# Optimization experiments

Measured on AMD Instinct MI355X. Metric: run time of the kernel, lower is better.

## Reference

```python
import jax, jax.numpy as jnp
import numpy as np

K = 3       # kernel_size
RATE = 2    # dilation rate
NH = 8      # num_heads
EPS = 1e-5  # InstanceNorm eps


def _conv1x1(x, W, b):
    # x: [B,C,H,W], W: [O,C], b: [O]
    return jnp.einsum('bchw,oc->bohw', x, W) + b[None, :, None, None]


def _inorm(x):
    mu = jnp.mean(x, axis=(2, 3), keepdims=True)
    var = jnp.var(x, axis=(2, 3), keepdims=True)
    return (x - mu) / jnp.sqrt(var + EPS)


def _extract_patches(x):
    # dilated KxK patches, stride 1, 'same' grid -> [B, C, K*K, H, W]
    B, C, H, W = x.shape
    pad = RATE * (K - 1) // 2
    xp = jnp.pad(x, ((0, 0), (0, 0), (pad, pad), (pad, pad)))
    taps = [xp[:, :, i * RATE:i * RATE + H, j * RATE:j * RATE + W]
            for i in range(K) for j in range(K)]
    return jnp.stack(taps, axis=2)


def setup_inputs() -> dict:
    key = jax.random.key(0)
    ks = jax.random.split(key, 8)
    B, C, H, W, A = 1, 64, 64, 64, 128
    features = jax.random.normal(ks[0], (B, C, H, W), jnp.float32)
    masks = jax.random.uniform(ks[1], (B, 1, H, W), jnp.float32)
    s_in = 1.0 / np.sqrt(C).astype(np.float32)
    Wq = jax.random.normal(ks[2], (A, C), jnp.float32) * s_in
    bq = jnp.zeros((A,), jnp.float32)
    Wk = jax.random.normal(ks[3], (A, C), jnp.float32) * s_in
    bk = jnp.zeros((A,), jnp.float32)
    Wo = jax.random.normal(ks[4], (C, C), jnp.float32) * s_in
    bo = jnp.zeros((C,), jnp.float32)
    return dict(features=features, masks=masks, Wq=Wq, bq=bq,
                Wk=Wk, bk=bk, Wo=Wo, bo=bo)


def reference(features, masks, Wq, bq, Wk, bk, Wo, bo):
    B, C, H, W = features.shape
    A = Wq.shape[0]
    hc = A // NH
    L = H * W
    KK = K * K

    m = (masks > 0.5).astype(features.dtype)          # 1 = hole
    f_masked = features * m
    f_unmasked = features * (1.0 - m)

    q = jax.nn.relu(_inorm(_conv1x1(f_masked, Wq, bq)))    # [B,A,H,W]
    k = jax.nn.relu(_inorm(_conv1x1(f_unmasked, Wk, bk)))  # [B,A,H,W]

    # per-head dilated patch banks: [B,NH,hc*KK,L]
    qp = _extract_patches(q).reshape(B, NH, hc * KK, L)
    kp = _extract_patches(k).reshape(B, NH, hc * KK, L)

    # patch-correlation attention per head: [B,NH,L,L]
    attn = jax.nn.softmax(jnp.einsum('bndq,bndk->bnqk', qp, kp), axis=-1)

    # value patch bank from unmasked features: [B,C*KK,L]
    vp = _extract_patches(f_unmasked).reshape(B, C * KK, L)

    # sample value patches: [B,NH,L,C*KK]
    sampled = jnp.einsum('bnqk,bdk->bnqd', attn, vp)

    # fold: average the KK taps per channel, then average over heads
    attended = sampled.reshape(B, NH, L, C, KK).mean(axis=4).mean(axis=1)  # [B,L,C]
    attended = attended.transpose(0, 2, 1).reshape(B, C, H, W)

    return jax.nn.relu(_inorm(_conv1x1(attended, Wo, bo)))
```

## Files before the change

### kernel.cpp

```cpp
#include <hip/hip_runtime.h>
#include <hip/hip_bf16.h>


#define LL 4096
#define CC 64
#define AA 128
#define NH_ 8
#define KSTR 144
#define LOG2E 1.44269504088896340736f

typedef _Float16 half8 __attribute__((ext_vector_type(8)));
typedef float floatx4 __attribute__((ext_vector_type(4)));
typedef int intx4 __attribute__((ext_vector_type(4)));

__device__ __forceinline__ float fexp2(float x) {
    float r;
    asm("v_exp_f32 %0, %1" : "=v"(r) : "v"(x));
    return r;
}

__global__ __launch_bounds__(512) void prep_kernel(
    const float* __restrict__ feat,
    const float* __restrict__ masks,
    const float* __restrict__ Wq, const float* __restrict__ bq,
    const float* __restrict__ Wk, const float* __restrict__ bk,
    _Float16* __restrict__ q_act, _Float16* __restrict__ k_act,
    _Float16* __restrict__ vb)
{
    const int tid = threadIdx.x;
    const int b = blockIdx.x;
    __shared__ float sWq[CC], sWk[CC];
    __shared__ float sm[32];

    if (b >= AA) {
        int c = b - AA;
        for (int p = 0; p < 8; ++p) {
            int l = p * 512 + tid;
            int y = l >> 6, x = l & 63;
            float s = 0.f;
            for (int ty = 0; ty < 3; ++ty) {
                int yy = y + 2 * (ty - 1);
                if (yy < 0 || yy > 63) continue;
                for (int tx = 0; tx < 3; ++tx) {
                    int xx = x + 2 * (tx - 1);
                    if (xx < 0 || xx > 63) continue;
                    int ll = yy * 64 + xx;
                    float hole = masks[ll] > 0.5f ? 1.f : 0.f;
                    s += feat[c * LL + ll] * (1.f - hole);
                }
            }
            vb[c * LL + l] = (_Float16)(s * (1.f / 9.f));
        }
        return;
    }

    const int a = b;
    if (tid < CC) {
        sWq[tid] = Wq[a * CC + tid];
        sWk[tid] = Wk[a * CC + tid];
    }
    __syncthreads();
    const float biasq = bq[a], biask = bk[a];

    float accq[8], acck[8];
#pragma unroll
    for (int p = 0; p < 8; ++p) { accq[p] = 0.f; acck[p] = 0.f; }
    for (int c = 0; c < CC; ++c) {
        float wq = sWq[c], wk = sWk[c];
        const float* fr = feat + (size_t)c * LL + tid;
#pragma unroll
        for (int p = 0; p < 8; ++p) {
            float f = fr[p * 512];
            accq[p] += wq * f;
            acck[p] += wk * f;
        }
    }

    float valsq[8], valsk[8];
    float s1q = 0.f, s2q = 0.f, s1k = 0.f, s2k = 0.f;
#pragma unroll
    for (int p = 0; p < 8; ++p) {
        int l = p * 512 + tid;
        float hole = masks[l] > 0.5f ? 1.f : 0.f;
        float vq = accq[p] * hole + biasq;
        float vk = acck[p] * (1.f - hole) + biask;
        valsq[p] = vq; s1q += vq; s2q += vq * vq;
        valsk[p] = vk; s1k += vk; s2k += vk * vk;
    }
    for (int off = 32; off; off >>= 1) {
        s1q += __shfl_down(s1q, off, 64);
        s2q += __shfl_down(s2q, off, 64);
        s1k += __shfl_down(s1k, off, 64);
        s2k += __shfl_down(s2k, off, 64);
    }
    int wv = tid >> 6, ln = tid & 63;
    if (ln == 0) {
        sm[wv * 4] = s1q; sm[wv * 4 + 1] = s2q;
        sm[wv * 4 + 2] = s1k; sm[wv * 4 + 3] = s2k;
    }
    __syncthreads();
    s1q = 0.f; s2q = 0.f; s1k = 0.f; s2k = 0.f;
#pragma unroll
    for (int i = 0; i < 8; ++i) {
        s1q += sm[i * 4]; s2q += sm[i * 4 + 1];
        s1k += sm[i * 4 + 2]; s2k += sm[i * 4 + 3];
    }
    float muq = s1q * (1.f / LL);
    float invq = rsqrtf(s2q * (1.f / LL) - muq * muq + 1e-5f);
    float muk = s1k * (1.f / LL);
    float invk = rsqrtf(s2k * (1.f / LL) - muk * muk + 1e-5f);

    _Float16* qa = q_act + (size_t)a * LL;
    _Float16* ka = k_act + (size_t)a * LL;
#pragma unroll
    for (int p = 0; p < 8; ++p) {
        int l = p * 512 + tid;
        float vq = (valsq[p] - muq) * invq;
        float vk = (valsk[p] - muk) * invk;
        qa[l] = (_Float16)(vq > 0.f ? vq * LOG2E : 0.f);
        ka[l] = (_Float16)(vk > 0.f ? vk : 0.f);
    }
}

__global__ __launch_bounds__(256) void build_kp(
    const _Float16* __restrict__ k_act, _Float16* __restrict__ kp)
{
    const int n = blockIdx.x, y = blockIdx.y;
    const int tid = threadIdx.x;
    const _Float16* ka = k_act + (size_t)n * 16 * LL;
    __shared__ _Float16 kt[16][3][72];

    for (int idx = tid; idx < 16 * 3 * 68; idx += 256) {
        int row = idx / 68, xr = idx - row * 68;
        int ah = row / 3, ty = row - ah * 3;
        int yy = y + 2 * (ty - 1);
        int xx = xr - 2;
        _Float16 v = (_Float16)0.f;
        if (yy >= 0 && yy <= 63 && xx >= 0 && xx <= 63)
            v = ka[ah * LL + yy * 64 + xx];
        kt[ah][ty][xr] = v;
    }
    __syncthreads();

    _Float16* base = kp + ((size_t)n * LL + y * 64) * KSTR;
#pragma unroll
    for (int i = 0; i < 5; ++i) {
        int idx = tid + i * 256;
        if (idx < 64 * 18) {
            int x = idx / 18, c18 = idx - x * 18;
            half8 v8;
#pragma unroll
            for (int j = 0; j < 8; ++j) {
                int d = c18 * 8 + j;
                int ah = d / 9, t = d - ah * 9;
                int ty = t / 3, tx = t - ty * 3;
                v8[j] = kt[ah][ty][x + 2 * tx];
            }
            *(half8*)(base + (size_t)idx * 8) = v8;
        }
    }
}

__global__ __launch_bounds__(256, 2) void attn_kernel(
    const _Float16* __restrict__ q_act, const _Float16* __restrict__ kp,
    const _Float16* __restrict__ vb,
    _Float16* __restrict__ Opart, float* __restrict__ ml)
{
    const int bid = blockIdx.x;
    const int n = bid & 7;
    const int slot = bid >> 3;
    const int qt2 = slot & 31;
    const int h = slot >> 5;
    const int jt0 = h * 32;
    const int tid = threadIdx.x;
    const int w = tid >> 6, lane = tid & 63;
    const int l15 = lane & 15, quad = lane >> 4;

    __shared__ __align__(16) _Float16 Bk[2][64 * KSTR + 16];

    if (tid < 32) Bk[tid >> 4][64 * KSTR + (tid & 15)] = (_Float16)0.f;

    const _Float16* kpn = kp + (size_t)n * LL * KSTR;

    auto issue_bk = [&](int jt, _Float16* dst) {
        const char* tile = (const char*)(kpn + (size_t)jt * 64 * KSTR) + (lane << 4);
        for (int c = w; c < 18; c += 4) {
            __builtin_amdgcn_global_load_lds(
                (const __attribute__((address_space(1))) void*)(tile + c * 1024),
                (__attribute__((address_space(3))) void*)(dst + c * 512),
                16, 0, 0);
        }
    };

    half8 afrag[2][5];
    {
        const _Float16* qa = q_act + (size_t)n * 16 * LL;
        const int x = w * 16 + l15;
#pragma unroll
        for (int rs = 0; rs < 2; ++rs) {
            const int y = qt2 * 2 + rs;
#pragma unroll
            for (int ks = 0; ks < 5; ++ks) {
#pragma unroll
                for (int j = 0; j < 8; ++j) {
                    int d = ks * 32 + quad * 8 + j;
                    _Float16 v = (_Float16)0.f;
                    if (d < 144) {
                        int ah = d / 9, t = d - ah * 9;
                        int ty = t / 3, tx = t - ty * 3;
                        int yy = y + 2 * (ty - 1);
                        int xx = x + 2 * (tx - 1);
                        if (yy >= 0 && yy <= 63 && xx >= 0 && xx <= 63)
                            v = qa[ah * LL + yy * 64 + xx];
                    }
                    afrag[rs][ks][j] = v;
                }
            }
        }
    }

    floatx4 accO[2][4];
    float mrow[2], lrow[2];
#pragma unroll
    for (int rs = 0; rs < 2; ++rs) {
        mrow[rs] = -1e30f; lrow[rs] = 0.f;
#pragma unroll
        for (int i = 0; i < 4; ++i) accO[rs][i] = (floatx4){0.f, 0.f, 0.f, 0.f};
    }

    const int aLo = (((quad & 1) << 5) + l15) << 2;
    const int aHi = aLo + 64;
    const bool selHi = (quad >> 1) != 0;

    const _Float16* vpl = vb + (size_t)l15 * LL + quad * 8;

    auto softmax_pack = [&](floatx4* accS, floatx4* accOr,
                            float& mr, float& lr, half8* pfr) {
        float t0 = fmaxf(fmaxf(accS[0][0], accS[0][1]), fmaxf(accS[0][2], accS[0][3]));
        float t1 = fmaxf(fmaxf(accS[1][0], accS[1][1]), fmaxf(accS[1][2], accS[1][3]));
        float t2 = fmaxf(fmaxf(accS[2][0], accS[2][1]), fmaxf(accS[2][2], accS[2][3]));
        float t3 = fmaxf(fmaxf(accS[3][0], accS[3][1]), fmaxf(accS[3][2], accS[3][3]));
        float tm = fmaxf(fmaxf(t0, t1), fmaxf(t2, t3));
        tm = fmaxf(tm, __shfl_xor(tm, 16, 64));
        tm = fmaxf(tm, __shfl_xor(tm, 32, 64));
        float mn = fmaxf(mr, tm);
        float alpha = fexp2(mr - mn);
        mr = mn;
        lr *= alpha;
        float af[4];
#pragma unroll
        for (int r = 0; r < 4; ++r) af[r] = __shfl(alpha, quad * 4 + r, 16);
#pragma unroll
        for (int nt = 0; nt < 4; ++nt)
#pragma unroll
            for (int r = 0; r < 4; ++r) accOr[nt][r] *= af[r];
        float rsum = 0.f;
#pragma unroll
        for (int nt = 0; nt < 4; ++nt)
#pragma unroll
            for (int r = 0; r < 4; ++r) {
                float pv = fexp2(accS[nt][r] - mn);
                accS[nt][r] = pv;
                rsum += pv;
            }
        lr += rsum;

        int pkw[4][2];
#pragma unroll
        for (int nt = 0; nt < 4; ++nt)
#pragma unroll
            for (int rp = 0; rp < 2; ++rp) {
                auto hp = __builtin_amdgcn_cvt_pkrtz(accS[nt][2 * rp],
                                                     accS[nt][2 * rp + 1]);
                pkw[nt][rp] = __builtin_bit_cast(int, hp);
            }
#pragma unroll
        for (int ks2 = 0; ks2 < 2; ++ks2) {
            int w0A = __builtin_amdgcn_ds_bpermute(aLo, pkw[2 * ks2][0]);
            int w0B = __builtin_amdgcn_ds_bpermute(aLo, pkw[2 * ks2 + 1][0]);
            int w1A = __builtin_amdgcn_ds_bpermute(aLo, pkw[2 * ks2][1]);
            int w1B = __builtin_amdgcn_ds_bpermute(aLo, pkw[2 * ks2 + 1][1]);
            int w2A = __builtin_amdgcn_ds_bpermute(aHi, pkw[2 * ks2][0]);
            int w2B = __builtin_amdgcn_ds_bpermute(aHi, pkw[2 * ks2 + 1][0]);
            int w3A = __builtin_amdgcn_ds_bpermute(aHi, pkw[2 * ks2][1]);
            int w3B = __builtin_amdgcn_ds_bpermute(aHi, pkw[2 * ks2 + 1][1]);
            intx4 wvv;
            wvv[0] = selHi ? w0B : w0A;
            wvv[1] = selHi ? w1B : w1A;
            wvv[2] = selHi ? w2B : w2A;
            wvv[3] = selHi ? w3B : w3A;
            pfr[ks2] = __builtin_bit_cast(half8, wvv);
        }
    };

    issue_bk(jt0, Bk[0]);

    int cur = 0;
    for (int it = 0; it < 32; ++it) {
        __syncthreads();

        if (it < 31) issue_bk(jt0 + it + 1, Bk[cur ^ 1]);

        const _Float16* vp = vpl + (jt0 + it) * 64;
        half8 vfrag[4][2];
#pragma unroll
        for (int nt = 0; nt < 4; ++nt)
#pragma unroll
            for (int ks2 = 0; ks2 < 2; ++ks2)
                vfrag[nt][ks2] = *(const half8*)(vp + (size_t)nt * 16 * LL + ks2 * 32);

        const _Float16* bk = Bk[cur];

        floatx4 accS0[4], accS1[4];
#pragma unroll
        for (int i = 0; i < 4; ++i) {
            accS0[i] = (floatx4){0.f, 0.f, 0.f, 0.f};
            accS1[i] = (floatx4){0.f, 0.f, 0.f, 0.f};
        }
        for (int ks = 0; ks < 5; ++ks) {
#pragma unroll
            for (int nt = 0; nt < 4; ++nt) {
                half8 bfr = *(const half8*)(bk + (nt * 16 + l15) * KSTR + ks * 32 + quad * 8);
                accS0[nt] = __builtin_amdgcn_mfma_f32_16x16x32_f16(bfr, afrag[0][ks], accS0[nt], 0, 0, 0);
                accS1[nt] = __builtin_amdgcn_mfma_f32_16x16x32_f16(bfr, afrag[1][ks], accS1[nt], 0, 0, 0);
            }
        }

        half8 pfr0[2], pfr1[2];
        softmax_pack(accS0, accO[0], mrow[0], lrow[0], pfr0);
#pragma unroll
        for (int ks2 = 0; ks2 < 2; ++ks2)
#pragma unroll
            for (int nt = 0; nt < 4; ++nt)
                accO[0][nt] = __builtin_amdgcn_mfma_f32_16x16x32_f16(pfr0[ks2], vfrag[nt][ks2], accO[0][nt], 0, 0, 0);

        softmax_pack(accS1, accO[1], mrow[1], lrow[1], pfr1);
#pragma unroll
        for (int ks2 = 0; ks2 < 2; ++ks2)
#pragma unroll
            for (int nt = 0; nt < 4; ++nt)
                accO[1][nt] = __builtin_amdgcn_mfma_f32_16x16x32_f16(pfr1[ks2], vfrag[nt][ks2], accO[1][nt], 0, 0, 0);

        cur ^= 1;
    }

#pragma unroll
    for (int rs = 0; rs < 2; ++rs) {
        const int y = qt2 * 2 + rs;
        float rsum = lrow[rs];
        rsum += __shfl_xor(rsum, 16, 64);
        rsum += __shfl_xor(rsum, 32, 64);
        float invl = 1.f / rsum;
        float iv[4];
#pragma unroll
        for (int r = 0; r < 4; ++r) iv[r] = __shfl(invl, quad * 4 + r, 16);

        _Float16* op = Opart + ((size_t)(n * 2 + h) * LL + y * 64 + w * 16) * CC;
#pragma unroll
        for (int r = 0; r < 4; ++r)
#pragma unroll
            for (int nt = 0; nt < 4; ++nt)
                op[(quad * 4 + r) * CC + nt * 16 + l15] = (_Float16)(accO[rs][nt][r] * iv[r]);

        if (quad == 0) {
            float* mlp = ml + ((size_t)n * LL + y * 64 + w * 16 + l15) * 4;
            mlp[2 * h] = mrow[rs];
            mlp[2 * h + 1] = rsum;
        }
    }
}

__global__ __launch_bounds__(256) void combine_kernel(
    const _Float16* __restrict__ Opart, const float* __restrict__ ml,
    float* __restrict__ att)
{
    int t = blockIdx.x * 256 + threadIdx.x;
    int l = t >> 6, c = t & 63;
    float s = 0.f;
#pragma unroll
    for (int n = 0; n < NH_; ++n) {
        const float* mlp = ml + ((size_t)n * LL + l) * 4;
        float m0 = mlp[0], l0 = mlp[1], m1 = mlp[2], l1 = mlp[3];
        float M = fmaxf(m0, m1);
        float w0 = l0 * fexp2(m0 - M);
        float w1 = l1 * fexp2(m1 - M);
        float o0 = (float)Opart[((size_t)(2 * n) * LL + l) * CC + c];
        float o1 = (float)Opart[((size_t)(2 * n + 1) * LL + l) * CC + c];
        s += (w0 * o0 + w1 * o1) / (w0 + w1);
    }
    att[t] = s * 0.125f;
}

__global__ __launch_bounds__(1024) void out_kernel(
    const float* __restrict__ att,
    const float* __restrict__ Wo, const float* __restrict__ bo,
    float* __restrict__ out)
{
    const int o = blockIdx.x;
    const int tid = threadIdx.x;
    __shared__ float sW[CC];
    __shared__ float sm[32];
    if (tid < CC) sW[tid] = Wo[o * CC + tid];
    __syncthreads();
    const float bias = bo[o];

    float vals[4], s1 = 0.f, s2 = 0.f;
#pragma unroll
    for (int p = 0; p < 4; ++p) {
        int l = p * 1024 + tid;
        const float4* arow = (const float4*)(att + (size_t)l * CC);
        float acc = bias;
#pragma unroll
        for (int c4 = 0; c4 < 16; ++c4) {
            float4 a4 = arow[c4];
            acc += sW[c4 * 4] * a4.x + sW[c4 * 4 + 1] * a4.y +
                   sW[c4 * 4 + 2] * a4.z + sW[c4 * 4 + 3] * a4.w;
        }
        vals[p] = acc; s1 += acc; s2 += acc * acc;
    }
    for (int off = 32; off; off >>= 1) {
        s1 += __shfl_down(s1, off, 64);
        s2 += __shfl_down(s2, off, 64);
    }
    int wv = tid >> 6, ln = tid & 63;
    if (ln == 0) { sm[wv * 2] = s1; sm[wv * 2 + 1] = s2; }
    __syncthreads();
    s1 = 0.f; s2 = 0.f;
#pragma unroll
    for (int i = 0; i < 16; ++i) { s1 += sm[2 * i]; s2 += sm[2 * i + 1]; }
    float mu = s1 * (1.f / LL);
    float inv = rsqrtf(s2 * (1.f / LL) - mu * mu + 1e-5f);
#pragma unroll
    for (int p = 0; p < 4; ++p) {
        int l = p * 1024 + tid;
        float v = (vals[p] - mu) * inv;
        out[(size_t)o * LL + l] = v > 0.f ? v : 0.f;
    }
}

extern "C" void kernel_launch(void* const* d_in, const int* in_sizes, int n_in,
                              void* d_out, int out_size, void* d_ws, size_t ws_size,
                              hipStream_t stream) {
    const float* feat  = (const float*)d_in[0];
    const float* masks = (const float*)d_in[1];
    const float* Wq    = (const float*)d_in[2];
    const float* bq    = (const float*)d_in[3];
    const float* Wk    = (const float*)d_in[4];
    const float* bk    = (const float*)d_in[5];
    const float* Wo    = (const float*)d_in[6];
    const float* bo    = (const float*)d_in[7];
    float* out = (float*)d_out;

    char* ws = (char*)d_ws;
    _Float16* q_act = (_Float16*)ws;
    _Float16* k_act = (_Float16*)(ws + 1048576);
    _Float16* vb    = (_Float16*)(ws + 2097152);
    float*    att   = (float*)(ws + 2621440);
    _Float16* kp    = (_Float16*)(ws + 3670016);
    _Float16* Opart = (_Float16*)(ws + 13107200);
    float*    ml    = (float*)(ws + 21495808);

    prep_kernel<<<AA + CC, 512, 0, stream>>>(feat, masks, Wq, bq, Wk, bk,
                                             q_act, k_act, vb);
    dim3 gb(NH_, 64);
    build_kp<<<gb, 256, 0, stream>>>(k_act, kp);
    attn_kernel<<<512, 256, 0, stream>>>(q_act, kp, vb, Opart, ml);
    combine_kernel<<<LL * CC / 256, 256, 0, stream>>>(Opart, ml, att);
    out_kernel<<<CC, 1024, 0, stream>>>(att, Wo, bo, out);
}
```

Before: 230.0 us.

## Process one query row per attention block and double the grid

Each attention block now handles a single query row instead of two, so the grid doubles from 512 to 1024 blocks. The K tile loaded into shared memory is now reused across one row instead of two, which doubles total K/V traffic. In return there are more blocks to fill the GPU and fewer live registers per thread. The V fragment loads also move after the QK^T MFMAs and softmax, which may hide their latency differently.

```diff
diff --git a/kernel.cpp b/kernel.cpp
--- a/kernel.cpp
+++ b/kernel.cpp
@@ -168,9 +168,9 @@
 {
     const int bid = blockIdx.x;
     const int n = bid & 7;
-    const int slot = bid >> 3;
-    const int qt2 = slot & 31;
-    const int h = slot >> 5;
+    const int rest = bid >> 3;
+    const int qt = rest & 63;
+    const int h = rest >> 6;
     const int jt0 = h * 32;
     const int tid = threadIdx.x;
     const int w = tid >> 6, lane = tid & 63;
@@ -192,41 +192,33 @@
         }
     };
 
-    half8 afrag[2][5];
+    half8 afrag[5];
     {
         const _Float16* qa = q_act + (size_t)n * 16 * LL;
         const int x = w * 16 + l15;
 #pragma unroll
-        for (int rs = 0; rs < 2; ++rs) {
-            const int y = qt2 * 2 + rs;
-#pragma unroll
-            for (int ks = 0; ks < 5; ++ks) {
-#pragma unroll
-                for (int j = 0; j < 8; ++j) {
-                    int d = ks * 32 + quad * 8 + j;
-                    _Float16 v = (_Float16)0.f;
-                    if (d < 144) {
-                        int ah = d / 9, t = d - ah * 9;
-                        int ty = t / 3, tx = t - ty * 3;
-                        int yy = y + 2 * (ty - 1);
-                        int xx = x + 2 * (tx - 1);
-                        if (yy >= 0 && yy <= 63 && xx >= 0 && xx <= 63)
-                            v = qa[ah * LL + yy * 64 + xx];
-                    }
-                    afrag[rs][ks][j] = v;
+        for (int ks = 0; ks < 5; ++ks) {
+#pragma unroll
+            for (int j = 0; j < 8; ++j) {
+                int d = ks * 32 + quad * 8 + j;
+                _Float16 v = (_Float16)0.f;
+                if (d < 144) {
+                    int ah = d / 9, t = d - ah * 9;
+                    int ty = t / 3, tx = t - ty * 3;
+                    int yy = qt + 2 * (ty - 1);
+                    int xx = x + 2 * (tx - 1);
+                    if (yy >= 0 && yy <= 63 && xx >= 0 && xx <= 63)
+                        v = qa[ah * LL + yy * 64 + xx];
                 }
-            }
-        }
-    }
-
-    floatx4 accO[2][4];
-    float mrow[2], lrow[2];
-#pragma unroll
-    for (int rs = 0; rs < 2; ++rs) {
-        mrow[rs] = -1e30f; lrow[rs] = 0.f;
-#pragma unroll
-        for (int i = 0; i < 4; ++i) accO[rs][i] = (floatx4){0.f, 0.f, 0.f, 0.f};
-    }
+                afrag[ks][j] = v;
+            }
+        }
+    }
+
+    floatx4 accO[4];
+    float mrow = -1e30f, lrow = 0.f;
+#pragma unroll
+    for (int i = 0; i < 4; ++i) accO[i] = (floatx4){0.f, 0.f, 0.f, 0.f};
 
     const int aLo = (((quad & 1) << 5) + l15) << 2;
     const int aHi = aLo + 64;
@@ -234,8 +226,27 @@
 
     const _Float16* vpl = vb + (size_t)l15 * LL + quad * 8;
 
-    auto softmax_pack = [&](floatx4* accS, floatx4* accOr,
-                            float& mr, float& lr, half8* pfr) {
+    issue_bk(jt0, Bk[0]);
+
+    int cur = 0;
+    for (int it = 0; it < 32; ++it) {
+        __syncthreads();
+
+        if (it < 31) issue_bk(jt0 + it + 1, Bk[cur ^ 1]);
+
+        const _Float16* bk = Bk[cur];
+
+        floatx4 accS[4];
+#pragma unroll
+        for (int i = 0; i < 4; ++i) accS[i] = (floatx4){0.f, 0.f, 0.f, 0.f};
+        for (int ks = 0; ks < 5; ++ks) {
+#pragma unroll
+            for (int nt = 0; nt < 4; ++nt) {
+                half8 bfr = *(const half8*)(bk + (nt * 16 + l15) * KSTR + ks * 32 + quad * 8);
+                accS[nt] = __builtin_amdgcn_mfma_f32_16x16x32_f16(bfr, afrag[ks], accS[nt], 0, 0, 0);
+            }
+        }
+
         float t0 = fmaxf(fmaxf(accS[0][0], accS[0][1]), fmaxf(accS[0][2], accS[0][3]));
         float t1 = fmaxf(fmaxf(accS[1][0], accS[1][1]), fmaxf(accS[1][2], accS[1][3]));
         float t2 = fmaxf(fmaxf(accS[2][0], accS[2][1]), fmaxf(accS[2][2], accS[2][3]));
@@ -243,17 +254,17 @@
         float tm = fmaxf(fmaxf(t0, t1), fmaxf(t2, t3));
         tm = fmaxf(tm, __shfl_xor(tm, 16, 64));
         tm = fmaxf(tm, __shfl_xor(tm, 32, 64));
-        float mn = fmaxf(mr, tm);
-        float alpha = fexp2(mr - mn);
-        mr = mn;
-        lr *= alpha;
+        float mn = fmaxf(mrow, tm);
+        float alpha = fexp2(mrow - mn);
+        mrow = mn;
+        lrow *= alpha;
         float af[4];
 #pragma unroll
         for (int r = 0; r < 4; ++r) af[r] = __shfl(alpha, quad * 4 + r, 16);
 #pragma unroll
         for (int nt = 0; nt < 4; ++nt)
 #pragma unroll
-            for (int r = 0; r < 4; ++r) accOr[nt][r] *= af[r];
+            for (int r = 0; r < 4; ++r) accO[nt][r] *= af[r];
         float rsum = 0.f;
 #pragma unroll
         for (int nt = 0; nt < 4; ++nt)
@@ -263,7 +274,15 @@
                 accS[nt][r] = pv;
                 rsum += pv;
             }
-        lr += rsum;
+        lrow += rsum;
+
+        const _Float16* vp = vpl + (jt0 + it) * 64;
+        half8 vfrag[4][2];
+#pragma unroll
+        for (int nt = 0; nt < 4; ++nt)
+#pragma unroll
+            for (int ks2 = 0; ks2 < 2; ++ks2)
+                vfrag[nt][ks2] = *(const half8*)(vp + (size_t)nt * 16 * LL + ks2 * 32);
 
         int pkw[4][2];
 #pragma unroll
@@ -274,6 +293,7 @@
                                                      accS[nt][2 * rp + 1]);
                 pkw[nt][rp] = __builtin_bit_cast(int, hp);
             }
+        half8 pfr[2];
 #pragma unroll
         for (int ks2 = 0; ks2 < 2; ++ks2) {
             int w0A = __builtin_amdgcn_ds_bpermute(aLo, pkw[2 * ks2][0]);
@@ -291,63 +311,18 @@
             wvv[3] = selHi ? w3B : w3A;
             pfr[ks2] = __builtin_bit_cast(half8, wvv);
         }
-    };
-
-    issue_bk(jt0, Bk[0]);
-
-    int cur = 0;
-    for (int it = 0; it < 32; ++it) {
-        __syncthreads();
-
-        if (it < 31) issue_bk(jt0 + it + 1, Bk[cur ^ 1]);
-
-        const _Float16* vp = vpl + (jt0 + it) * 64;
-        half8 vfrag[4][2];
-#pragma unroll
-        for (int nt = 0; nt < 4; ++nt)
-#pragma unroll
-            for (int ks2 = 0; ks2 < 2; ++ks2)
-                vfrag[nt][ks2] = *(const half8*)(vp + (size_t)nt * 16 * LL + ks2 * 32);
-
-        const _Float16* bk = Bk[cur];
-
-        floatx4 accS0[4], accS1[4];
-#pragma unroll
-        for (int i = 0; i < 4; ++i) {
-            accS0[i] = (floatx4){0.f, 0.f, 0.f, 0.f};
-            accS1[i] = (floatx4){0.f, 0.f, 0.f, 0.f};
-        }
-        for (int ks = 0; ks < 5; ++ks) {
-#pragma unroll
-            for (int nt = 0; nt < 4; ++nt) {
-                half8 bfr = *(const half8*)(bk + (nt * 16 + l15) * KSTR + ks * 32 + quad * 8);
-                accS0[nt] = __builtin_amdgcn_mfma_f32_16x16x32_f16(bfr, afrag[0][ks], accS0[nt], 0, 0, 0);
-                accS1[nt] = __builtin_amdgcn_mfma_f32_16x16x32_f16(bfr, afrag[1][ks], accS1[nt], 0, 0, 0);
-            }
-        }
-
-        half8 pfr0[2], pfr1[2];
-        softmax_pack(accS0, accO[0], mrow[0], lrow[0], pfr0);
+
 #pragma unroll
         for (int ks2 = 0; ks2 < 2; ++ks2)
 #pragma unroll
             for (int nt = 0; nt < 4; ++nt)
-                accO[0][nt] = __builtin_amdgcn_mfma_f32_16x16x32_f16(pfr0[ks2], vfrag[nt][ks2], accO[0][nt], 0, 0, 0);
-
-        softmax_pack(accS1, accO[1], mrow[1], lrow[1], pfr1);
-#pragma unroll
-        for (int ks2 = 0; ks2 < 2; ++ks2)
-#pragma unroll
-            for (int nt = 0; nt < 4; ++nt)
-                accO[1][nt] = __builtin_amdgcn_mfma_f32_16x16x32_f16(pfr1[ks2], vfrag[nt][ks2], accO[1][nt], 0, 0, 0);
+                accO[nt] = __builtin_amdgcn_mfma_f32_16x16x32_f16(pfr[ks2], vfrag[nt][ks2], accO[nt], 0, 0, 0);
 
         cur ^= 1;
     }
 
-#pragma unroll
-    for (int rs = 0; rs < 2; ++rs) {
-        const int y = qt2 * 2 + rs;
-        float rsum = lrow[rs];
+    {
+        float rsum = lrow;
         rsum += __shfl_xor(rsum, 16, 64);
         rsum += __shfl_xor(rsum, 32, 64);
         float invl = 1.f / rsum;
@@ -355,16 +330,16 @@
 #pragma unroll
         for (int r = 0; r < 4; ++r) iv[r] = __shfl(invl, quad * 4 + r, 16);
 
-        _Float16* op = Opart + ((size_t)(n * 2 + h) * LL + y * 64 + w * 16) * CC;
+        _Float16* op = Opart + ((size_t)(n * 2 + h) * LL + qt * 64 + w * 16) * CC;
 #pragma unroll
         for (int r = 0; r < 4; ++r)
 #pragma unroll
             for (int nt = 0; nt < 4; ++nt)
-                op[(quad * 4 + r) * CC + nt * 16 + l15] = (_Float16)(accO[rs][nt][r] * iv[r]);
+                op[(quad * 4 + r) * CC + nt * 16 + l15] = (_Float16)(accO[nt][r] * iv[r]);
 
         if (quad == 0) {
-            float* mlp = ml + ((size_t)n * LL + y * 64 + w * 16 + l15) * 4;
-            mlp[2 * h] = mrow[rs];
+            float* mlp = ml + ((size_t)n * LL + qt * 64 + w * 16 + l15) * 4;
+            mlp[2 * h] = mrow;
             mlp[2 * h + 1] = rsum;
         }
     }
@@ -464,7 +439,7 @@
                                              q_act, k_act, vb);
     dim3 gb(NH_, 64);
     build_kp<<<gb, 256, 0, stream>>>(k_act, kp);
-    attn_kernel<<<512, 256, 0, stream>>>(q_act, kp, vb, Opart, ml);
+    attn_kernel<<<1024, 256, 0, stream>>>(q_act, kp, vb, Opart, ml);
     combine_kernel<<<LL * CC / 256, 256, 0, stream>>>(Opart, ml, att);
     out_kernel<<<CC, 1024, 0, stream>>>(att, Wo, bo, out);
 }
```

Result: slower. 293.0 us (+27.4%).
